# Kernel optimization log

Measured on AMD Instinct MI355X. Metric: run time of the kernel, lower is better.

## Reference

```python
import jax, jax.numpy as jnp
import numpy as np

NUM_USERS = 100000
NUM_ITEMS = 50000
EMBED_K = 64
N_LAYERS = 3
FEAT = 1024
N_EDGES = 3000000
BATCH = 16384


def setup_inputs() -> dict:
    key = jax.random.key(0)
    ks = jax.random.split(key, 10)
    Gu = 0.1 * jax.random.normal(ks[0], (NUM_USERS, EMBED_K), jnp.float32)
    Gi = 0.1 * jax.random.normal(ks[1], (NUM_ITEMS, EMBED_K), jnp.float32)
    Tu = jax.random.normal(ks[2], (NUM_USERS, EMBED_K), jnp.float32) * (6.0 / (NUM_USERS + EMBED_K)) ** 0.5
    F = jax.random.normal(ks[3], (NUM_ITEMS, FEAT), jnp.float32)
    proj_w = jax.random.normal(ks[4], (EMBED_K, FEAT), jnp.float32) * (1.0 / FEAT) ** 0.5
    proj_b = jnp.zeros((EMBED_K,), jnp.float32)
    user_edges = jax.random.randint(ks[5], (N_EDGES,), 0, NUM_USERS, jnp.int32)
    item_edges = jax.random.randint(ks[6], (N_EDGES,), 0, NUM_ITEMS, jnp.int32)
    users = jax.random.randint(ks[7], (BATCH,), 0, NUM_USERS, jnp.int32)
    items = jax.random.randint(ks[8], (BATCH,), 0, NUM_ITEMS, jnp.int32)
    return {"Gu": Gu, "Gi": Gi, "Tu": Tu, "F": F, "proj_w": proj_w, "proj_b": proj_b,
            "user_edges": user_edges, "item_edges": item_edges, "users": users, "items": items}


def _propagate(Gu, Gi, src, dst, n_layers):
    # LightGCN: n_layers of symmetric-normalized LGConv, then mean over [x0..xL]
    N = Gu.shape[0] + Gi.shape[0]
    deg = jax.ops.segment_sum(jnp.ones_like(src, jnp.float32), dst, num_segments=N)
    dinv = jnp.where(deg > 0, jax.lax.rsqrt(jnp.maximum(deg, 1.0)), 0.0)
    norm = dinv[src] * dinv[dst]  # [2E]
    x = jnp.concatenate([Gu, Gi], axis=0)  # [N, K]
    acc = x
    for _ in range(n_layers):
        x = jax.ops.segment_sum(x[src] * norm[:, None], dst, num_segments=N)
        acc = acc + x
    all_emb = acc / (n_layers + 1)
    return all_emb[:Gu.shape[0]], all_emb[Gu.shape[0]:]


def reference(Gu, Gi, Tu, F, proj_w, proj_b, user_edges, item_edges, users, items):
    nu = Gu.shape[0]
    # symmetric bipartite edges: user->item and item->user
    src = jnp.concatenate([user_edges, item_edges + nu])
    dst = jnp.concatenate([item_edges + nu, user_edges])
    gu, gi = _propagate(Gu, Gi, src, dst, N_LAYERS)
    gamma_u = gu[users]          # [B, K]
    gamma_i = gi[items]          # [B, K]
    theta_u = Tu[users]          # [B, K]
    proj = F[items] @ proj_w.T + proj_b  # [B, K]
    proj_i = proj / jnp.maximum(jnp.linalg.norm(proj, axis=1, keepdims=True), 1e-12)
    xui = jnp.sum(gamma_u * gamma_i, axis=1) + jnp.sum(theta_u * proj_i, axis=1)
    return xui
```

## Files before the change

kernel.cpp:

```cpp
#include <hip/hip_runtime.h>
#include <hip/hip_bf16.h>
#include <hip/hip_fp16.h>


#define WAVE 64
#define NBMAX 592
#define SLOTS 14336
#define ETG 1792

typedef int nt_int4 __attribute__((ext_vector_type(4)));

__device__ __forceinline__ unsigned pack2(float lo, float hi) {
    __half2 h = __floats2half2_rn(lo, hi);
    return *(unsigned*)&h;
}
__device__ __forceinline__ float2 unpack2(unsigned u) {
    __half2 h = *(__half2*)&u;
    return __half22float2(h);
}

__global__ __launch_bounds__(256) void bhist_kernel(const int* __restrict__ ue,
                                                    const int* __restrict__ ie,
                                                    int* __restrict__ bcnt,
                                                    int E, int nu, int NB, int shift,
                                                    int gpb, int NG) {
    __shared__ int lh[NBMAX];
    int tid = threadIdx.x;
    for (int b = tid; b < NB; b += 256) lh[b] = 0;
    __syncthreads();
    int g0 = blockIdx.x * gpb;
    int g1 = min(g0 + gpb, NG);
    for (int g = g0 + tid; g < g1; g += 256) {
        int e0 = g * 4;
        if (e0 + 3 < E) {
            nt_int4 u = __builtin_nontemporal_load((const nt_int4*)(ue + e0));
            nt_int4 v = __builtin_nontemporal_load((const nt_int4*)(ie + e0));
            atomicAdd(&lh[(nu + v.x) >> shift], 1); atomicAdd(&lh[u.x >> shift], 1);
            atomicAdd(&lh[(nu + v.y) >> shift], 1); atomicAdd(&lh[u.y >> shift], 1);
            atomicAdd(&lh[(nu + v.z) >> shift], 1); atomicAdd(&lh[u.z >> shift], 1);
            atomicAdd(&lh[(nu + v.w) >> shift], 1); atomicAdd(&lh[u.w >> shift], 1);
        } else {
            for (int e = e0; e < E; ++e) {
                atomicAdd(&lh[(nu + ie[e]) >> shift], 1);
                atomicAdd(&lh[ue[e] >> shift], 1);
            }
        }
    }
    __syncthreads();
    for (int b = tid; b < NB; b += 256) if (lh[b]) atomicAdd(&bcnt[b], lh[b]);
}

__global__ __launch_bounds__(1024) void bscan_kernel(const int* __restrict__ bcnt,
                                                     int* __restrict__ pbase,
                                                     int* __restrict__ pcur, int NB) {
    __shared__ int wsum[16];
    int t = threadIdx.x;
    int v0 = (t < NB) ? bcnt[t] : 0;
    int lane = t & 63, w = t >> 6;
    int v = v0;
    #pragma unroll
    for (int d = 1; d < 64; d <<= 1) {
        int o = __shfl_up(v, d, 64);
        if (lane >= d) v += o;
    }
    if (lane == 63) wsum[w] = v;
    __syncthreads();
    if (t == 0) {
        int r = 0;
        #pragma unroll
        for (int k = 0; k < 16; ++k) { int s = wsum[k]; wsum[k] = r; r += s; }
    }
    __syncthreads();
    int excl = (v - v0) + wsum[w];
    if (t < NB) { pbase[t] = excl; pcur[t] = excl; }
}

__global__ __launch_bounds__(256) void scatter_kernel(const int* __restrict__ ue,
                                                      const int* __restrict__ ie,
                                                      int* __restrict__ pcur,
                                                      int* __restrict__ pairs,
                                                      int E, int nu, int shift,
                                                      int NB, int NG) {
    __shared__ int slot[SLOTS];
    __shared__ int lhist[NBMAX];
    __shared__ int lcur[NBMAX];
    __shared__ int gbase[NBMAX];
    int tid = threadIdx.x;
    for (int b = tid; b < NB; b += 256) lhist[b] = 0;
    __syncthreads();
    int g0 = blockIdx.x * ETG;
    int g1 = min(g0 + ETG, NG);
    int mask = (1 << shift) - 1;
    for (int g = g0 + tid; g < g1; g += 256) {
        int e0 = g * 4;
        if (e0 + 3 < E) {
            nt_int4 u = __builtin_nontemporal_load((const nt_int4*)(ue + e0));
            nt_int4 v = __builtin_nontemporal_load((const nt_int4*)(ie + e0));
            atomicAdd(&lhist[(nu + v.x) >> shift], 1); atomicAdd(&lhist[u.x >> shift], 1);
            atomicAdd(&lhist[(nu + v.y) >> shift], 1); atomicAdd(&lhist[u.y >> shift], 1);
            atomicAdd(&lhist[(nu + v.z) >> shift], 1); atomicAdd(&lhist[u.z >> shift], 1);
            atomicAdd(&lhist[(nu + v.w) >> shift], 1); atomicAdd(&lhist[u.w >> shift], 1);
        } else {
            for (int e = e0; e < E; ++e) {
                atomicAdd(&lhist[(nu + ie[e]) >> shift], 1);
                atomicAdd(&lhist[ue[e] >> shift], 1);
            }
        }
    }
    __syncthreads();
    if (tid < 64) {
        int carry = 0;
        for (int c = 0; c < NB; c += 64) {
            int idx = c + tid;
            int x = (idx < NB) ? lhist[idx] : 0;
            int v = x;
            #pragma unroll
            for (int d = 1; d < 64; d <<= 1) {
                int o = __shfl_up(v, d, 64);
                if (tid >= d) v += o;
            }
            if (idx < NB) lcur[idx] = v - x + carry;
            carry += __shfl(v, 63, 64);
        }
    }
    __syncthreads();
    for (int b = tid; b < NB; b += 256) {
        int c = lhist[b];
        if (c) gbase[b] = atomicAdd(&pcur[b], c);
    }
    for (int g = g0 + tid; g < g1; g += 256) {
        int e0 = g * 4;
        if (e0 + 3 < E) {
            nt_int4 u = __builtin_nontemporal_load((const nt_int4*)(ue + e0));
            nt_int4 v = __builtin_nontemporal_load((const nt_int4*)(ie + e0));
            int uu[4] = {u.x, u.y, u.z, u.w};
            int vv[4] = {nu + v.x, nu + v.y, nu + v.z, nu + v.w};
            #pragma unroll
            for (int t = 0; t < 4; ++t) {
                int d = vv[t], s = uu[t];
                int p = atomicAdd(&lcur[d >> shift], 1);
                slot[p] = ((d & mask) << 18) | s;
                d = uu[t]; s = vv[t];
                p = atomicAdd(&lcur[d >> shift], 1);
                slot[p] = ((d & mask) << 18) | s;
            }
        } else {
            for (int e = e0; e < E; ++e) {
                int d = nu + ie[e], s = ue[e];
                int p = atomicAdd(&lcur[d >> shift], 1);
                slot[p] = ((d & mask) << 18) | s;
                d = ue[e]; s = nu + ie[e];
                p = atomicAdd(&lcur[d >> shift], 1);
                slot[p] = ((d & mask) << 18) | s;
            }
        }
    }
    __syncthreads();
    int w = tid >> 6, lane = tid & 63;
    for (int b = w; b < NB; b += 4) {
        int c = lhist[b];
        if (!c) continue;
        int start = lcur[b] - c;
        int gb = gbase[b];
        for (int i = lane; i < c; i += 64)
            pairs[gb + i] = slot[start + i];
    }
}

__global__ __launch_bounds__(256) void build_kernel(const int* __restrict__ pairs,
                                                    const int* __restrict__ pbase,
                                                    const int* __restrict__ pcur,
                                                    int* __restrict__ offs,
                                                    float* __restrict__ dinv,
                                                    float* __restrict__ drt,
                                                    int* __restrict__ col,
                                                    int N, int shift, int NB, int twoE) {
    __shared__ int dcnt[512];
    __shared__ int ex[512];
    __shared__ int cur[512];
    int b = blockIdx.x, tid = threadIdx.x;
    int lo = b << shift;
    int n = min(1 << shift, N - lo);
    for (int i = tid; i < 512; i += 256) dcnt[i] = 0;
    __syncthreads();
    int pb = pbase[b];
    int cnt = pcur[b] - pb;
    for (int i = tid; i < cnt; i += 256) {
        int p = pairs[pb + i];
        atomicAdd(&dcnt[p >> 18], 1);
    }
    __syncthreads();
    if (tid < 64) {
        int base = tid * 8;
        int loc[8]; int s = 0;
        #pragma unroll
        for (int k = 0; k < 8; ++k) { loc[k] = s; s += dcnt[base + k]; }
        int v = s;
        #pragma unroll
        for (int d = 1; d < 64; d <<= 1) {
            int o = __shfl_up(v, d, 64);
            if (tid >= d) v += o;
        }
        int excl = v - s;
        #pragma unroll
        for (int k = 0; k < 8; ++k) ex[base + k] = excl + loc[k];
    }
    __syncthreads();
    for (int i = tid; i < n; i += 256) {
        int c = pb + ex[i];
        cur[i] = c;
        offs[lo + i] = c;
        int d = dcnt[i];
        dinv[lo + i] = (d > 0) ? rsqrtf((float)d) : 0.0f;
        drt[lo + i]  = (d > 0) ? sqrtf((float)d)  : 0.0f;
    }
    if (b == NB - 1 && tid == 0) offs[N] = twoE;
    __syncthreads();
    for (int i = tid; i < cnt; i += 256) {
        int p = pairs[pb + i];
        int pos = atomicAdd(&cur[p >> 18], 1);
        col[pos] = p & 0x3FFFF;
    }
}

__global__ void mark_kernel(const int* __restrict__ users, const int* __restrict__ items,
                            int* __restrict__ flag, int B, int nu) {
    int b = blockIdx.x * blockDim.x + threadIdx.x;
    if (b < B) {
        flag[users[b]] = 1;
        flag[nu + items[b]] = 1;
    }
}

__global__ void compact_kernel(const int* __restrict__ flag, int* __restrict__ list,
                               int* __restrict__ cnt, int N) {
    int n = blockIdx.x * blockDim.x + threadIdx.x;
    if (n < N && flag[n]) {
        int pos = atomicAdd(cnt, 1);
        list[pos] = n;
    }
}

__global__ void init_z_kernel(const float* __restrict__ Gu, const float* __restrict__ Gi,
                              const float* __restrict__ dinv,
                              __half* __restrict__ z, int nu, int N) {
    int id = blockIdx.x * blockDim.x + threadIdx.x;
    if (id < N * 8) {
        int n = id >> 3, q = id & 7;
        const float4* src = (n < nu) ? (const float4*)Gu : (const float4*)Gi;
        int j = (n < nu) ? n : n - nu;
        float4 a0 = src[(size_t)j * 16 + q * 2];
        float4 a1 = src[(size_t)j * 16 + q * 2 + 1];
        float w = dinv[n];
        uint4 o;
        o.x = pack2(a0.x * w, a0.y * w);
        o.y = pack2(a0.z * w, a0.w * w);
        o.z = pack2(a1.x * w, a1.y * w);
        o.w = pack2(a1.z * w, a1.w * w);
        ((uint4*)z)[id] = o;
    }
}

__global__ void init_bacc_kernel(const float* __restrict__ Gu, const float* __restrict__ Gi,
                                 const int* __restrict__ users, const int* __restrict__ items,
                                 float* __restrict__ baccU, float* __restrict__ baccI, int B) {
    int id = blockIdx.x * blockDim.x + threadIdx.x;
    if (id < B * 16) {
        int b = id >> 4, q = id & 15;
        ((float4*)baccU)[id] = ((const float4*)Gu)[(size_t)users[b] * 16 + q];
        ((float4*)baccI)[id] = ((const float4*)Gi)[(size_t)items[b] * 16 + q];
    }
}

__global__ __launch_bounds__(256) void pull_kernel(const __half* __restrict__ z,
                                                   __half* __restrict__ zn,
                                                   const int* __restrict__ offs,
                                                   const int* __restrict__ col,
                                                   const float* __restrict__ dinv,
                                                   const int* __restrict__ rows,
                                                   const int* __restrict__ n_ptr, int N) {
    int wid = (blockIdx.x * blockDim.x + threadIdx.x) >> 6;
    int lane = threadIdx.x & 63;
    int nrows = rows ? *n_ptr : N;
    if (wid >= nrows) return;
    int r = rows ? rows[wid] : wid;
    int s = offs[r], e = offs[r + 1];
    int slot = lane >> 3;
    int q    = lane & 7;
    float a0 = 0.f, a1 = 0.f, a2 = 0.f, a3 = 0.f;
    float a4 = 0.f, a5 = 0.f, a6 = 0.f, a7 = 0.f;
    for (int base = s; base < e; base += 64) {
        int idx = base + lane;
        int c = (idx < e) ? __builtin_nontemporal_load(col + idx) : 0;
        int n = min(64, e - base);
        int nfull = n & ~7;
        int j = 0;
        for (; j < nfull; j += 8) {
            int cj = __shfl(c, j + slot);
            uint4 v = ((const uint4*)(z + (size_t)cj * WAVE))[q];
            float2 f0 = unpack2(v.x), f1 = unpack2(v.y);
            float2 f2 = unpack2(v.z), f3 = unpack2(v.w);
            a0 += f0.x; a1 += f0.y; a2 += f1.x; a3 += f1.y;
            a4 += f2.x; a5 += f2.y; a6 += f3.x; a7 += f3.y;
        }
        if (j < n) {
            int take = n - j;
            int cj = __shfl(c, j + (slot < take ? slot : 0));
            uint4 v = ((const uint4*)(z + (size_t)cj * WAVE))[q];
            if (slot < take) {
                float2 f0 = unpack2(v.x), f1 = unpack2(v.y);
                float2 f2 = unpack2(v.z), f3 = unpack2(v.w);
                a0 += f0.x; a1 += f0.y; a2 += f1.x; a3 += f1.y;
                a4 += f2.x; a5 += f2.y; a6 += f3.x; a7 += f3.y;
            }
        }
    }
    #pragma unroll
    for (int d = 8; d < 64; d <<= 1) {
        a0 += __shfl_xor(a0, d, 64); a1 += __shfl_xor(a1, d, 64);
        a2 += __shfl_xor(a2, d, 64); a3 += __shfl_xor(a3, d, 64);
        a4 += __shfl_xor(a4, d, 64); a5 += __shfl_xor(a5, d, 64);
        a6 += __shfl_xor(a6, d, 64); a7 += __shfl_xor(a7, d, 64);
    }
    if (slot == 0) {
        float w = dinv[r];
        float ww = w * w;
        uint4 o;
        o.x = pack2(a0 * ww, a1 * ww);
        o.y = pack2(a2 * ww, a3 * ww);
        o.z = pack2(a4 * ww, a5 * ww);
        o.w = pack2(a6 * ww, a7 * ww);
        ((uint4*)(zn + (size_t)r * WAVE))[q] = o;
    }
}

__global__ void gather_acc_kernel(const __half* __restrict__ zn,
                                  const float* __restrict__ drt,
                                  const int* __restrict__ users, const int* __restrict__ items,
                                  float* __restrict__ baccU, float* __restrict__ baccI,
                                  int B, int nu) {
    int id = blockIdx.x * blockDim.x + threadIdx.x;
    if (id < B * 8) {
        int b = id >> 3, q = id & 7;
        int u = users[b], it = nu + items[b];
        float wu = drt[u], wi = drt[it];
        uint4 vu = ((const uint4*)(zn))[(size_t)u * 8 + q];
        uint4 vi = ((const uint4*)(zn))[(size_t)it * 8 + q];
        float2 u0 = unpack2(vu.x), u1 = unpack2(vu.y), u2 = unpack2(vu.z), u3 = unpack2(vu.w);
        float2 i0 = unpack2(vi.x), i1 = unpack2(vi.y), i2 = unpack2(vi.z), i3 = unpack2(vi.w);
        float4* bu = (float4*)baccU + (size_t)b * 16 + q * 2;
        float4* bi = (float4*)baccI + (size_t)b * 16 + q * 2;
        float4 a = bu[0];
        a.x += wu * u0.x; a.y += wu * u0.y; a.z += wu * u1.x; a.w += wu * u1.y;
        bu[0] = a;
        a = bu[1];
        a.x += wu * u2.x; a.y += wu * u2.y; a.z += wu * u3.x; a.w += wu * u3.y;
        bu[1] = a;
        a = bi[0];
        a.x += wi * i0.x; a.y += wi * i0.y; a.z += wi * i1.x; a.w += wi * i1.y;
        bi[0] = a;
        a = bi[1];
        a.x += wi * i2.x; a.y += wi * i2.y; a.z += wi * i3.x; a.w += wi * i3.y;
        bi[1] = a;
    }
}

__global__ __launch_bounds__(256) void proj_out_kernel(const float* __restrict__ baccU,
                                                       const float* __restrict__ baccI,
                                                       const float* __restrict__ Tu,
                                                       const float* __restrict__ F,
                                                       const float* __restrict__ W,
                                                       const float* __restrict__ bvec,
                                                       const int* __restrict__ users,
                                                       const int* __restrict__ items,
                                                       float* __restrict__ out,
                                                       int B, float invL) {
    const int FEATn = 1024;
    __shared__ float Ft[2][32][64];
    __shared__ float Wt[2][32][64];

    int tid = threadIdx.x;
    int tx = tid & 15;
    int ty = tid >> 4;
    int r0 = blockIdx.x * 64;

    int lr = tid >> 2;
    int lq = tid & 3;
    int frow = min(r0 + lr, B - 1);
    const float* Fp = F + (size_t)items[frow] * FEATn + lq * 4;
    const float* Wp = W + (size_t)lr * FEATn + lq * 4;

    float4 fa0 = *(const float4*)(Fp);
    float4 fa1 = *(const float4*)(Fp + 16);
    float4 wa0 = *(const float4*)(Wp);
    float4 wa1 = *(const float4*)(Wp + 16);

    float acc[4][4] = {};

    for (int kt = 0; kt < 32; ++kt) {
        int buf = kt & 1;
        #pragma unroll
        for (int i = 0; i < 4; ++i) {
            Ft[buf][lq * 4 + i][lr]      = ((const float*)&fa0)[i];
            Ft[buf][lq * 4 + 16 + i][lr] = ((const float*)&fa1)[i];
            Wt[buf][lq * 4 + i][lr]      = ((const float*)&wa0)[i];
            Wt[buf][lq * 4 + 16 + i][lr] = ((const float*)&wa1)[i];
        }
        __syncthreads();
        if (kt < 31) {
            const float* fp = Fp + (kt + 1) * 32;
            const float* wp = Wp + (kt + 1) * 32;
            fa0 = *(const float4*)(fp);
            fa1 = *(const float4*)(fp + 16);
            wa0 = *(const float4*)(wp);
            wa1 = *(const float4*)(wp + 16);
        }
        #pragma unroll 8
        for (int kk = 0; kk < 32; ++kk) {
            float4 a = *(const float4*)&Ft[buf][kk][ty * 4];
            float4 b = *(const float4*)&Wt[buf][kk][tx * 4];
            acc[0][0] = fmaf(a.x, b.x, acc[0][0]);
            acc[0][1] = fmaf(a.x, b.y, acc[0][1]);
            acc[0][2] = fmaf(a.x, b.z, acc[0][2]);
            acc[0][3] = fmaf(a.x, b.w, acc[0][3]);
            acc[1][0] = fmaf(a.y, b.x, acc[1][0]);
            acc[1][1] = fmaf(a.y, b.y, acc[1][1]);
            acc[1][2] = fmaf(a.y, b.z, acc[1][2]);
            acc[1][3] = fmaf(a.y, b.w, acc[1][3]);
            acc[2][0] = fmaf(a.z, b.x, acc[2][0]);
            acc[2][1] = fmaf(a.z, b.y, acc[2][1]);
            acc[2][2] = fmaf(a.z, b.z, acc[2][2]);
            acc[2][3] = fmaf(a.z, b.w, acc[2][3]);
            acc[3][0] = fmaf(a.w, b.x, acc[3][0]);
            acc[3][1] = fmaf(a.w, b.y, acc[3][1]);
            acc[3][2] = fmaf(a.w, b.z, acc[3][2]);
            acc[3][3] = fmaf(a.w, b.w, acc[3][3]);
        }
    }

    float4 bb = *(const float4*)(bvec + tx * 4);
    float L2 = invL * invL;
    float res[4];
    #pragma unroll
    for (int r = 0; r < 4; ++r) {
        int gr = min(r0 + ty * 4 + r, B - 1);
        float pb0 = acc[r][0] + bb.x;
        float pb1 = acc[r][1] + bb.y;
        float pb2 = acc[r][2] + bb.z;
        float pb3 = acc[r][3] + bb.w;
        float s = pb0 * pb0 + pb1 * pb1 + pb2 * pb2 + pb3 * pb3;
        #pragma unroll
        for (int d = 1; d < 16; d <<= 1) s += __shfl_xor(s, d, 64);
        float inv = 1.0f / fmaxf(sqrtf(s), 1e-12f);
        int u = users[gr];
        float4 tu = *(const float4*)(Tu + (size_t)u * WAVE + tx * 4);
        float4 gu = *(const float4*)(baccU + (size_t)gr * WAVE + tx * 4);
        float4 gi = *(const float4*)(baccI + (size_t)gr * WAVE + tx * 4);
        float dsum = L2 * (gu.x * gi.x + gu.y * gi.y + gu.z * gi.z + gu.w * gi.w)
                   + inv * (tu.x * pb0 + tu.y * pb1 + tu.z * pb2 + tu.w * pb3);
        #pragma unroll
        for (int d = 1; d < 16; d <<= 1) dsum += __shfl_xor(dsum, d, 64);
        res[r] = dsum;
    }
    if (tx == 0) {
        #pragma unroll
        for (int r = 0; r < 4; ++r) {
            int gr = r0 + ty * 4 + r;
            if (gr < B) out[gr] = res[r];
        }
    }
}

extern "C" void kernel_launch(void* const* d_in, const int* in_sizes, int n_in,
                              void* d_out, int out_size, void* d_ws, size_t ws_size,
                              hipStream_t stream) {
    const float* Gu = (const float*)d_in[0];
    const float* Gi = (const float*)d_in[1];
    const float* Tu = (const float*)d_in[2];
    const float* F  = (const float*)d_in[3];
    const float* W  = (const float*)d_in[4];
    const float* bv = (const float*)d_in[5];
    const int* ue    = (const int*)d_in[6];
    const int* ie    = (const int*)d_in[7];
    const int* users = (const int*)d_in[8];
    const int* items = (const int*)d_in[9];
    float* out = (float*)d_out;

    const int K  = 64;
    const int nu = in_sizes[0] / K;
    const int ni = in_sizes[1] / K;
    const int N  = nu + ni;
    const int E  = in_sizes[6];
    const int B  = in_sizes[8];

    char* p = (char*)d_ws;
    auto alloc = [&](size_t bytes) -> void* {
        void* r = (void*)p;
        p += (bytes + 255) & ~(size_t)255;
        return r;
    };
    float* dinv   = (float*)alloc((size_t)N * 4);
    float* drt    = (float*)alloc((size_t)N * 4);
    int*   offs   = (int*)  alloc((size_t)(N + 1) * 4);
    int*   flags  = (int*)  alloc((size_t)N * 4);
    int*   col    = (int*)  alloc((size_t)2 * E * 4);
    __half* za    = (__half*)alloc((size_t)N * K * 2);
    __half* zb    = (__half*)alloc((size_t)N * K * 2);
    float* baccU  = (float*)alloc((size_t)B * K * 4);
    float* baccI  = (float*)alloc((size_t)B * K * 4);
    int*   list   = (int*)  alloc((size_t)2 * B * 4);
    int*   cnt    = (int*)  alloc(256);
    int*   bcnt   = (int*)  alloc((size_t)NBMAX * 4);
    int*   pbase  = (int*)  alloc((size_t)NBMAX * 4);
    int*   pcur   = (int*)  alloc((size_t)NBMAX * 4);

    int shift = 8;
    while (((N + (1 << shift) - 1) >> shift) > NBMAX) ++shift;
    const int NB = (N + (1 << shift) - 1) >> shift;

    int* pairs = (int*)za;

    const int NG   = (E + 3) / 4;
    const int gpbH = (NG + 1023) / 1024;
    const int nbS  = (NG + ETG - 1) / ETG;

    hipMemsetAsync(bcnt, 0, (size_t)NB * 4, stream);
    bhist_kernel<<<1024, 256, 0, stream>>>(ue, ie, bcnt, E, nu, NB, shift, gpbH, NG);
    bscan_kernel<<<1, 1024, 0, stream>>>(bcnt, pbase, pcur, NB);
    scatter_kernel<<<nbS, 256, 0, stream>>>(ue, ie, pcur, pairs, E, nu, shift, NB, NG);
    build_kernel<<<NB, 256, 0, stream>>>(pairs, pbase, pcur, offs, dinv, drt, col,
                                         N, shift, NB, 2 * E);

    hipMemsetAsync(flags, 0, (size_t)N * 4, stream);
    hipMemsetAsync(cnt, 0, 4, stream);
    mark_kernel<<<(B + 255) / 256, 256, 0, stream>>>(users, items, flags, B, nu);
    compact_kernel<<<(N + 255) / 256, 256, 0, stream>>>(flags, list, cnt, N);

    init_z_kernel<<<(N * 8 + 255) / 256, 256, 0, stream>>>(Gu, Gi, dinv, za, nu, N);
    init_bacc_kernel<<<(B * 16 + 255) / 256, 256, 0, stream>>>(Gu, Gi, users, items,
                                                               baccU, baccI, B);

    pull_kernel<<<(N + 3) / 4, 256, 0, stream>>>(za, zb, offs, col, dinv,
                                                 nullptr, nullptr, N);
    gather_acc_kernel<<<(B * 8 + 255) / 256, 256, 0, stream>>>(zb, drt, users, items,
                                                               baccU, baccI, B, nu);
    pull_kernel<<<(N + 3) / 4, 256, 0, stream>>>(zb, za, offs, col, dinv,
                                                 nullptr, nullptr, N);
    gather_acc_kernel<<<(B * 8 + 255) / 256, 256, 0, stream>>>(za, drt, users, items,
                                                               baccU, baccI, B, nu);
    pull_kernel<<<(2 * B + 3) / 4, 256, 0, stream>>>(za, zb, offs, col, dinv,
                                                     list, cnt, N);
    gather_acc_kernel<<<(B * 8 + 255) / 256, 256, 0, stream>>>(zb, drt, users, items,
                                                               baccU, baccI, B, nu);

    proj_out_kernel<<<(B + 63) / 64, 256, 0, stream>>>(baccU, baccI, Tu, F, W, bv,
                                                       users, items, out, B, 0.25f);
}
```

Before: 732.8 us.

## Use per-block bucket histograms with column scan for deterministic edge placement

New measurement: 700.6 us. 4.4% less time.

```diff
diff --git a/kernel.cpp b/kernel.cpp
--- a/kernel.cpp
+++ b/kernel.cpp
@@ -19,78 +19,17 @@
     return __half22float2(h);
 }
 
-__global__ __launch_bounds__(256) void bhist_kernel(const int* __restrict__ ue,
+__global__ __launch_bounds__(256) void histA_kernel(const int* __restrict__ ue,
                                                     const int* __restrict__ ie,
-                                                    int* __restrict__ bcnt,
-                                                    int E, int nu, int NB, int shift,
-                                                    int gpb, int NG) {
-    __shared__ int lh[NBMAX];
-    int tid = threadIdx.x;
-    for (int b = tid; b < NB; b += 256) lh[b] = 0;
-    __syncthreads();
-    int g0 = blockIdx.x * gpb;
-    int g1 = min(g0 + gpb, NG);
-    for (int g = g0 + tid; g < g1; g += 256) {
-        int e0 = g * 4;
-        if (e0 + 3 < E) {
-            nt_int4 u = __builtin_nontemporal_load((const nt_int4*)(ue + e0));
-            nt_int4 v = __builtin_nontemporal_load((const nt_int4*)(ie + e0));
-            atomicAdd(&lh[(nu + v.x) >> shift], 1); atomicAdd(&lh[u.x >> shift], 1);
-            atomicAdd(&lh[(nu + v.y) >> shift], 1); atomicAdd(&lh[u.y >> shift], 1);
-            atomicAdd(&lh[(nu + v.z) >> shift], 1); atomicAdd(&lh[u.z >> shift], 1);
-            atomicAdd(&lh[(nu + v.w) >> shift], 1); atomicAdd(&lh[u.w >> shift], 1);
-        } else {
-            for (int e = e0; e < E; ++e) {
-                atomicAdd(&lh[(nu + ie[e]) >> shift], 1);
-                atomicAdd(&lh[ue[e] >> shift], 1);
-            }
-        }
-    }
-    __syncthreads();
-    for (int b = tid; b < NB; b += 256) if (lh[b]) atomicAdd(&bcnt[b], lh[b]);
-}
-
-__global__ __launch_bounds__(1024) void bscan_kernel(const int* __restrict__ bcnt,
-                                                     int* __restrict__ pbase,
-                                                     int* __restrict__ pcur, int NB) {
-    __shared__ int wsum[16];
-    int t = threadIdx.x;
-    int v0 = (t < NB) ? bcnt[t] : 0;
-    int lane = t & 63, w = t >> 6;
-    int v = v0;
-    #pragma unroll
-    for (int d = 1; d < 64; d <<= 1) {
-        int o = __shfl_up(v, d, 64);
-        if (lane >= d) v += o;
-    }
-    if (lane == 63) wsum[w] = v;
-    __syncthreads();
-    if (t == 0) {
-        int r = 0;
-        #pragma unroll
-        for (int k = 0; k < 16; ++k) { int s = wsum[k]; wsum[k] = r; r += s; }
-    }
-    __syncthreads();
-    int excl = (v - v0) + wsum[w];
-    if (t < NB) { pbase[t] = excl; pcur[t] = excl; }
-}
-
-__global__ __launch_bounds__(256) void scatter_kernel(const int* __restrict__ ue,
-                                                      const int* __restrict__ ie,
-                                                      int* __restrict__ pcur,
-                                                      int* __restrict__ pairs,
-                                                      int E, int nu, int shift,
-                                                      int NB, int NG) {
-    __shared__ int slot[SLOTS];
+                                                    int* __restrict__ bh,
+                                                    int E, int nu, int shift,
+                                                    int NB, int NG) {
     __shared__ int lhist[NBMAX];
-    __shared__ int lcur[NBMAX];
-    __shared__ int gbase[NBMAX];
     int tid = threadIdx.x;
     for (int b = tid; b < NB; b += 256) lhist[b] = 0;
     __syncthreads();
     int g0 = blockIdx.x * ETG;
     int g1 = min(g0 + ETG, NG);
-    int mask = (1 << shift) - 1;
     for (int g = g0 + tid; g < g1; g += 256) {
         int e0 = g * 4;
         if (e0 + 3 < E) {
@@ -108,6 +47,77 @@
         }
     }
     __syncthreads();
+    int* row = bh + (size_t)blockIdx.x * NB;
+    for (int b = tid; b < NB; b += 256) row[b] = lhist[b];
+}
+
+__global__ __launch_bounds__(64) void colscan_kernel(const int* __restrict__ bh,
+                                                     int* __restrict__ gb,
+                                                     int* __restrict__ tot,
+                                                     int NBLK, int NB) {
+    int b = blockIdx.x;
+    int lane = threadIdx.x;
+    int carry = 0;
+    for (int i0 = 0; i0 < NBLK; i0 += 64) {
+        int i = i0 + lane;
+        int x = (i < NBLK) ? bh[(size_t)i * NB + b] : 0;
+        int v = x;
+        #pragma unroll
+        for (int d = 1; d < 64; d <<= 1) {
+            int o = __shfl_up(v, d, 64);
+            if (lane >= d) v += o;
+        }
+        if (i < NBLK) gb[(size_t)i * NB + b] = v - x + carry;
+        carry += __shfl(v, 63, 64);
+    }
+    if (lane == 0) tot[b] = carry;
+}
+
+__global__ __launch_bounds__(1024) void bscan_kernel(const int* __restrict__ tot,
+                                                     int* __restrict__ pbase,
+                                                     int NB, int twoE) {
+    __shared__ int wsum[16];
+    int t = threadIdx.x;
+    int v0 = (t < NB) ? tot[t] : 0;
+    int lane = t & 63, w = t >> 6;
+    int v = v0;
+    #pragma unroll
+    for (int d = 1; d < 64; d <<= 1) {
+        int o = __shfl_up(v, d, 64);
+        if (lane >= d) v += o;
+    }
+    if (lane == 63) wsum[w] = v;
+    __syncthreads();
+    if (t == 0) {
+        int r = 0;
+        #pragma unroll
+        for (int k = 0; k < 16; ++k) { int s = wsum[k]; wsum[k] = r; r += s; }
+        pbase[NB] = twoE;
+    }
+    __syncthreads();
+    int excl = (v - v0) + wsum[w];
+    if (t < NB) pbase[t] = excl;
+}
+
+__global__ __launch_bounds__(256) void place_kernel(const int* __restrict__ ue,
+                                                    const int* __restrict__ ie,
+                                                    const int* __restrict__ bh,
+                                                    const int* __restrict__ gb,
+                                                    const int* __restrict__ pbase,
+                                                    int* __restrict__ pairs,
+                                                    int E, int nu, int shift,
+                                                    int NB, int NG) {
+    __shared__ int slot[SLOTS];
+    __shared__ int lhist[NBMAX];
+    __shared__ int lcur[NBMAX];
+    __shared__ int lbase[NBMAX];
+    int blk = blockIdx.x, tid = threadIdx.x;
+    for (int b = tid; b < NB; b += 256) {
+        int c = bh[(size_t)blk * NB + b];
+        lhist[b] = c;
+        lbase[b] = pbase[b] + gb[(size_t)blk * NB + b];
+    }
+    __syncthreads();
     if (tid < 64) {
         int carry = 0;
         for (int c = 0; c < NB; c += 64) {
@@ -124,10 +134,9 @@
         }
     }
     __syncthreads();
-    for (int b = tid; b < NB; b += 256) {
-        int c = lhist[b];
-        if (c) gbase[b] = atomicAdd(&pcur[b], c);
-    }
+    int g0 = blk * ETG;
+    int g1 = min(g0 + ETG, NG);
+    int mask = (1 << shift) - 1;
     for (int g = g0 + tid; g < g1; g += 256) {
         int e0 = g * 4;
         if (e0 + 3 < E) {
@@ -161,15 +170,14 @@
         int c = lhist[b];
         if (!c) continue;
         int start = lcur[b] - c;
-        int gb = gbase[b];
+        int gb0 = lbase[b];
         for (int i = lane; i < c; i += 64)
-            pairs[gb + i] = slot[start + i];
+            pairs[gb0 + i] = slot[start + i];
     }
 }
 
 __global__ __launch_bounds__(256) void build_kernel(const int* __restrict__ pairs,
                                                     const int* __restrict__ pbase,
-                                                    const int* __restrict__ pcur,
                                                     int* __restrict__ offs,
                                                     float* __restrict__ dinv,
                                                     float* __restrict__ drt,
@@ -184,7 +192,7 @@
     for (int i = tid; i < 512; i += 256) dcnt[i] = 0;
     __syncthreads();
     int pb = pbase[b];
-    int cnt = pcur[b] - pb;
+    int cnt = pbase[b + 1] - pb;
     for (int i = tid; i < cnt; i += 256) {
         int p = pairs[pb + i];
         atomicAdd(&dcnt[p >> 18], 1);
@@ -287,6 +295,7 @@
     int s = offs[r], e = offs[r + 1];
     int slot = lane >> 3;
     int q    = lane & 7;
+    const uint4* zq = (const uint4*)z;
     float a0 = 0.f, a1 = 0.f, a2 = 0.f, a3 = 0.f;
     float a4 = 0.f, a5 = 0.f, a6 = 0.f, a7 = 0.f;
     for (int base = s; base < e; base += 64) {
@@ -295,18 +304,28 @@
         int n = min(64, e - base);
         int nfull = n & ~7;
         int j = 0;
-        for (; j < nfull; j += 8) {
-            int cj = __shfl(c, j + slot);
-            uint4 v = ((const uint4*)(z + (size_t)cj * WAVE))[q];
+        if (nfull > 0) {
+            int cj = __shfl(c, slot);
+            uint4 v = zq[(size_t)cj * 8 + q];
+            for (j = 8; j < nfull; j += 8) {
+                int cn = __shfl(c, j + slot);
+                uint4 vn = zq[(size_t)cn * 8 + q];
+                float2 f0 = unpack2(v.x), f1 = unpack2(v.y);
+                float2 f2 = unpack2(v.z), f3 = unpack2(v.w);
+                a0 += f0.x; a1 += f0.y; a2 += f1.x; a3 += f1.y;
+                a4 += f2.x; a5 += f2.y; a6 += f3.x; a7 += f3.y;
+                v = vn;
+            }
             float2 f0 = unpack2(v.x), f1 = unpack2(v.y);
             float2 f2 = unpack2(v.z), f3 = unpack2(v.w);
             a0 += f0.x; a1 += f0.y; a2 += f1.x; a3 += f1.y;
             a4 += f2.x; a5 += f2.y; a6 += f3.x; a7 += f3.y;
+            j = nfull;
         }
         if (j < n) {
             int take = n - j;
             int cj = __shfl(c, j + (slot < take ? slot : 0));
-            uint4 v = ((const uint4*)(z + (size_t)cj * WAVE))[q];
+            uint4 v = zq[(size_t)cj * 8 + q];
             if (slot < take) {
                 float2 f0 = unpack2(v.x), f1 = unpack2(v.y);
                 float2 f2 = unpack2(v.z), f3 = unpack2(v.w);
@@ -493,6 +512,13 @@
     const int E  = in_sizes[6];
     const int B  = in_sizes[8];
 
+    int shift = 8;
+    while (((N + (1 << shift) - 1) >> shift) > NBMAX) ++shift;
+    const int NB = (N + (1 << shift) - 1) >> shift;
+
+    const int NG   = (E + 3) / 4;
+    const int nbS  = (NG + ETG - 1) / ETG;
+
     char* p = (char*)d_ws;
     auto alloc = [&](size_t bytes) -> void* {
         void* r = (void*)p;
@@ -510,25 +536,19 @@
     float* baccI  = (float*)alloc((size_t)B * K * 4);
     int*   list   = (int*)  alloc((size_t)2 * B * 4);
     int*   cnt    = (int*)  alloc(256);
-    int*   bcnt   = (int*)  alloc((size_t)NBMAX * 4);
-    int*   pbase  = (int*)  alloc((size_t)NBMAX * 4);
-    int*   pcur   = (int*)  alloc((size_t)NBMAX * 4);
-
-    int shift = 8;
-    while (((N + (1 << shift) - 1) >> shift) > NBMAX) ++shift;
-    const int NB = (N + (1 << shift) - 1) >> shift;
+    int*   bh     = (int*)  alloc((size_t)nbS * NB * 4);
+    int*   gb     = (int*)  alloc((size_t)nbS * NB * 4);
+    int*   tot    = (int*)  alloc((size_t)NBMAX * 4);
+    int*   pbase  = (int*)  alloc((size_t)(NBMAX + 1) * 4);
 
     int* pairs = (int*)za;
 
-    const int NG   = (E + 3) / 4;
-    const int gpbH = (NG + 1023) / 1024;
-    const int nbS  = (NG + ETG - 1) / ETG;
-
-    hipMemsetAsync(bcnt, 0, (size_t)NB * 4, stream);
-    bhist_kernel<<<1024, 256, 0, stream>>>(ue, ie, bcnt, E, nu, NB, shift, gpbH, NG);
-    bscan_kernel<<<1, 1024, 0, stream>>>(bcnt, pbase, pcur, NB);
-    scatter_kernel<<<nbS, 256, 0, stream>>>(ue, ie, pcur, pairs, E, nu, shift, NB, NG);
-    build_kernel<<<NB, 256, 0, stream>>>(pairs, pbase, pcur, offs, dinv, drt, col,
+    histA_kernel<<<nbS, 256, 0, stream>>>(ue, ie, bh, E, nu, shift, NB, NG);
+    colscan_kernel<<<NB, 64, 0, stream>>>(bh, gb, tot, nbS, NB);
+    bscan_kernel<<<1, 1024, 0, stream>>>(tot, pbase, NB, 2 * E);
+    place_kernel<<<nbS, 256, 0, stream>>>(ue, ie, bh, gb, pbase, pairs,
+                                          E, nu, shift, NB, NG);
+    build_kernel<<<NB, 256, 0, stream>>>(pairs, pbase, offs, dinv, drt, col,
                                          N, shift, NB, 2 * E);
 
     hipMemsetAsync(flags, 0, (size_t)N * 4, stream);
```
